# Kernel tuning notes

Hardware: AMD Instinct MI355X
Metric: run time of the kernel (lower is better)

Reference implementation:

```python
import jax, jax.numpy as jnp
import numpy as np

B, S, NQ, H, HD = 2, 4096, 576, 32, 128
HID = H * HD  # 4096


def setup_inputs() -> dict:
    key = jax.random.key(0)
    ks = jax.random.split(key, 7)
    sc = 0.02
    return {
        "hidden_states": jax.random.normal(ks[0], (B, S, HID), jnp.float32),
        "by_pass_hidden_states": jax.random.normal(ks[1], (B, NQ, HID), jnp.float32),
        "attention_mask": jnp.zeros((B, 1, S, NQ), jnp.float32),
        "Wq": jax.random.normal(ks[2], (HID, HID), jnp.float32) * sc,
        "Wk": jax.random.normal(ks[3], (HID, HID), jnp.float32) * sc,
        "Wv": jax.random.normal(ks[4], (HID, HID), jnp.float32) * sc,
        "Wo": jax.random.normal(ks[5], (HID, HID), jnp.float32) * sc,
    }


def reference(hidden_states, by_pass_hidden_states, attention_mask, Wq, Wk, Wv, Wo):
    b, s, _ = hidden_states.shape
    nq = by_pass_hidden_states.shape[1]
    # projections (nn.Linear applies x @ W.T); reshape to (b, heads, len, head_dim)
    q = (hidden_states @ Wq.T).reshape(b, s, H, HD).transpose(0, 2, 1, 3)
    k = (by_pass_hidden_states @ Wk.T).reshape(b, nq, H, HD).transpose(0, 2, 1, 3)
    v = (by_pass_hidden_states @ Wv.T).reshape(b, nq, H, HD).transpose(0, 2, 1, 3)
    # eager QK^T -> mask -> fp32 softmax -> V
    scores = jnp.einsum("bhsd,bhqd->bhsq", q, k) / jnp.sqrt(jnp.float32(HD))
    scores = scores + attention_mask  # (b,1,s,nq) broadcast over heads
    attn = jax.nn.softmax(scores.astype(jnp.float32), axis=-1).astype(q.dtype)
    out = jnp.einsum("bhsq,bhqd->bhsd", attn, v)
    out = out.transpose(0, 2, 1, 3).reshape(b, s, HID)
    return out @ Wo.T
```

## Files before the change

### kernel.cpp

```cpp
#include <hip/hip_runtime.h>
#include <stdint.h>

#define Bn   2
#define Sn   4096
#define NQn  576
#define Hn   32
#define HDn  128
#define HIDn 4096

typedef unsigned short bfu;
typedef short short8 __attribute__((ext_vector_type(8)));
typedef float f32x4 __attribute__((ext_vector_type(4)));

__device__ __forceinline__ bfu f2b(float f) {
  uint32_t x = __builtin_bit_cast(uint32_t, f);
  return (bfu)((x + 0x7fffu + ((x >> 16) & 1u)) >> 16);
}

__device__ __forceinline__ void gload16(const void* g, void* l) {
  __builtin_amdgcn_global_load_lds(
      (const __attribute__((address_space(1))) uint32_t*)g,
      (__attribute__((address_space(3))) uint32_t*)l, 16, 0, 0);
}

__global__ void cast_f32_bf16(const float* __restrict__ in, bfu* __restrict__ out,
                              int n8) {
  int i = blockIdx.x * 256 + threadIdx.x;
  if (i >= n8) return;
  const float4* in4 = (const float4*)in;
  float4 a = in4[2 * i], c = in4[2 * i + 1];
  short8 v;
  v[0] = (short)f2b(a.x); v[1] = (short)f2b(a.y);
  v[2] = (short)f2b(a.z); v[3] = (short)f2b(a.w);
  v[4] = (short)f2b(c.x); v[5] = (short)f2b(c.y);
  v[6] = (short)f2b(c.z); v[7] = (short)f2b(c.w);
  ((short8*)out)[i] = v;
}

template <int WRITE_BF16>
__global__ __launch_bounds__(512, 2)
void gemm_bt256(const bfu* __restrict__ A, const bfu* __restrict__ Bm,
                void* __restrict__ Cout, int M, int N, int K) {
  __shared__ __align__(16) bfu Asm[2][256 * 64];
  __shared__ __align__(16) bfu Bsm[2][256 * 64];
  const int tid = threadIdx.x;
  const int wave = tid >> 6, lane = tid & 63;
  const int lr = lane & 15, kq = lane >> 4;
  const int wm = wave >> 2, wn = wave & 3;
  const long m0 = (long)blockIdx.y * 256, n0 = (long)blockIdx.x * 256;
  const int NT = K >> 6;

  const int c0j = tid >> 3, c0c = tid & 7;
  const int c1j = (512 + tid) >> 3, c1c = tid & 7;
  const bfu* aSrc0 = A + (m0 + c0j) * (long)K + ((c0c ^ (c0j & 7)) * 8);
  const bfu* aSrc1 = A + (m0 + c1j) * (long)K + ((c1c ^ (c1j & 7)) * 8);
  const bfu* bSrc0 = Bm + (n0 + c0j) * (long)K + ((c0c ^ (c0j & 7)) * 8);
  const bfu* bSrc1 = Bm + (n0 + c1j) * (long)K + ((c1c ^ (c1j & 7)) * 8);

  auto stageA = [&](int t, int buf, int half) {
    long koff = (long)t * 64 + (long)half * 128 * K;
    gload16(aSrc0 + koff, &Asm[buf][half * 8192 + (wave * 64) * 8]);
    gload16(aSrc1 + koff, &Asm[buf][half * 8192 + (512 + wave * 64) * 8]);
  };
  auto stageB = [&](int t, int buf, int half) {
    long koff = (long)t * 64 + (long)half * 128 * K;
    gload16(bSrc0 + koff, &Bsm[buf][half * 8192 + (wave * 64) * 8]);
    gload16(bSrc1 + koff, &Bsm[buf][half * 8192 + (512 + wave * 64) * 8]);
  };
  auto ldsA = [&](int buf, int mf, int ks) -> short8 {
    int row = (mf >> 2) * 128 + wm * 64 + (mf & 3) * 16 + lr;
    int off = (row * 128 + ks * 64 + kq * 16) ^ ((row & 7) << 4);
    return *(const short8*)((const char*)Asm[buf] + off);
  };
  auto ldsB = [&](int buf, int nf, int ks) -> short8 {
    int row = (nf >> 1) * 128 + wn * 32 + (nf & 1) * 16 + lr;
    int off = (row * 128 + ks * 64 + kq * 16) ^ ((row & 7) << 4);
    return *(const short8*)((const char*)Bsm[buf] + off);
  };

  f32x4 acc[8][4] = {};

  stageA(0, 0, 0); stageB(0, 0, 0); stageB(0, 0, 1); stageA(0, 0, 1);
  asm volatile("s_waitcnt vmcnt(0)" ::: "memory");
  __builtin_amdgcn_s_barrier();

  for (int t = 0; t < NT; ++t) {
    const int buf = t & 1;
    if (t + 1 < NT) {
      stageA(t + 1, buf ^ 1, 0);
      stageB(t + 1, buf ^ 1, 0);
      stageB(t + 1, buf ^ 1, 1);
      stageA(t + 1, buf ^ 1, 1);
    }
    short8 a0[4][2], a1[4][2], b0[2][2], b1[2][2];
#pragma unroll
    for (int mf = 0; mf < 4; ++mf) {
      a0[mf][0] = ldsA(buf, mf, 0);
      a0[mf][1] = ldsA(buf, mf, 1);
    }
#pragma unroll
    for (int nf = 0; nf < 2; ++nf) {
      b0[nf][0] = ldsB(buf, nf, 0);
      b0[nf][1] = ldsB(buf, nf, 1);
      b1[nf][0] = ldsB(buf, 2 + nf, 0);
      b1[nf][1] = ldsB(buf, 2 + nf, 1);
    }
#pragma unroll
    for (int mf = 0; mf < 4; ++mf)
#pragma unroll
      for (int ks = 0; ks < 2; ++ks)
#pragma unroll
        for (int nf = 0; nf < 2; ++nf)
          acc[mf][nf] = __builtin_amdgcn_mfma_f32_16x16x32_bf16(
              a0[mf][ks], b0[nf][ks], acc[mf][nf], 0, 0, 0);
#pragma unroll
    for (int mf = 0; mf < 4; ++mf) {
      a1[mf][0] = ldsA(buf, 4 + mf, 0);
      a1[mf][1] = ldsA(buf, 4 + mf, 1);
    }
#pragma unroll
    for (int mf = 0; mf < 4; ++mf)
#pragma unroll
      for (int ks = 0; ks < 2; ++ks)
#pragma unroll
        for (int nf = 0; nf < 2; ++nf)
          acc[mf][2 + nf] = __builtin_amdgcn_mfma_f32_16x16x32_bf16(
              a0[mf][ks], b1[nf][ks], acc[mf][2 + nf], 0, 0, 0);
#pragma unroll
    for (int mf = 0; mf < 4; ++mf)
#pragma unroll
      for (int ks = 0; ks < 2; ++ks)
#pragma unroll
        for (int nf = 0; nf < 2; ++nf)
          acc[4 + mf][2 + nf] = __builtin_amdgcn_mfma_f32_16x16x32_bf16(
              a1[mf][ks], b1[nf][ks], acc[4 + mf][2 + nf], 0, 0, 0);
#pragma unroll
    for (int mf = 0; mf < 4; ++mf)
#pragma unroll
      for (int ks = 0; ks < 2; ++ks)
#pragma unroll
        for (int nf = 0; nf < 2; ++nf)
          acc[4 + mf][nf] = __builtin_amdgcn_mfma_f32_16x16x32_bf16(
              a1[mf][ks], b0[nf][ks], acc[4 + mf][nf], 0, 0, 0);
    asm volatile("s_waitcnt vmcnt(0)" ::: "memory");
    __builtin_amdgcn_s_barrier();
  }

#pragma unroll
  for (int mf = 0; mf < 8; ++mf)
#pragma unroll
    for (int nf = 0; nf < 4; ++nf)
#pragma unroll
      for (int r = 0; r < 4; ++r) {
        long row = m0 + (mf >> 2) * 128 + wm * 64 + (mf & 3) * 16 + kq * 4 + r;
        long col = n0 + (nf >> 1) * 128 + wn * 32 + (nf & 1) * 16 + lr;
        float v = acc[mf][nf][r];
        if (WRITE_BF16)
          ((bfu*)Cout)[row * N + col] = f2b(v);
        else
          ((float*)Cout)[row * N + col] = v;
      }
}

template <int WRITE_BF16>
__global__ __launch_bounds__(256, 2)
void gemm_bt(const bfu* __restrict__ A, const bfu* __restrict__ Bm,
             void* __restrict__ Cout, int M, int N, int K) {
  __shared__ __align__(16) bfu As[128 * 32];
  __shared__ __align__(16) bfu Bs[128 * 32];
  const int tid = threadIdx.x;
  const int wave = tid >> 6, lane = tid & 63;
  const int lr = lane & 15, kq = lane >> 4;
  const int wm = wave >> 1, wn = wave & 1;
  const long m0 = (long)blockIdx.y * 128, n0 = (long)blockIdx.x * 128;

  f32x4 acc[4][4] = {};

  for (int kk = 0; kk < K; kk += 32) {
#pragma unroll
    for (int i = 0; i < 2; ++i) {
      int tt = i * 256 + tid;
      long row = tt >> 2;
      int col = (tt & 3) * 8;
      gload16(A + (m0 + row) * K + kk + col, &As[(i * 256 + wave * 64) * 8]);
      gload16(Bm + (n0 + row) * K + kk + col, &Bs[(i * 256 + wave * 64) * 8]);
    }
    __syncthreads();
    short8 a[4], b[4];
#pragma unroll
    for (int mt = 0; mt < 4; ++mt)
      a[mt] = *(const short8*)&As[(wm * 64 + mt * 16 + lr) * 32 + kq * 8];
#pragma unroll
    for (int nt = 0; nt < 4; ++nt)
      b[nt] = *(const short8*)&Bs[(wn * 64 + nt * 16 + lr) * 32 + kq * 8];
#pragma unroll
    for (int mt = 0; mt < 4; ++mt)
#pragma unroll
      for (int nt = 0; nt < 4; ++nt)
        acc[mt][nt] = __builtin_amdgcn_mfma_f32_16x16x32_bf16(
            a[mt], b[nt], acc[mt][nt], 0, 0, 0);
    __syncthreads();
  }
#pragma unroll
  for (int mt = 0; mt < 4; ++mt)
#pragma unroll
    for (int nt = 0; nt < 4; ++nt)
#pragma unroll
      for (int r = 0; r < 4; ++r) {
        long row = m0 + wm * 64 + mt * 16 + kq * 4 + r;
        long col = n0 + wn * 64 + nt * 16 + lr;
        float v = acc[mt][nt][r];
        if (WRITE_BF16)
          ((bfu*)Cout)[row * N + col] = f2b(v);
        else
          ((float*)Cout)[row * N + col] = v;
      }
}

__global__ void transpose_v(const bfu* __restrict__ Vb, bfu* __restrict__ Vt) {
  __shared__ bfu t[32][33];
  const int bh = blockIdx.z;
  const int tq = blockIdx.x;
  const int td = blockIdx.y;
  const int b = bh >> 5, h = bh & 31;
  const int tx = threadIdx.x & 31, ty = threadIdx.x >> 5;
  const bfu* src = Vb + ((long)(b * NQn + tq * 32)) * HIDn + h * HDn + td * 32;
#pragma unroll
  for (int i = 0; i < 32; i += 8) t[ty + i][tx] = src[(long)(ty + i) * HIDn + tx];
  __syncthreads();
  bfu* dst = Vt + ((long)bh * HDn + td * 32) * NQn + tq * 32;
#pragma unroll
  for (int i = 0; i < 32; i += 8) dst[(long)(ty + i) * NQn + tx] = t[tx][ty + i];
}

__global__ __launch_bounds__(256, 3)
void attn_kernel(const bfu* __restrict__ Qb, const bfu* __restrict__ Kb,
                 const bfu* __restrict__ Vt, const float* __restrict__ mask,
                 bfu* __restrict__ AO) {
  __shared__ __align__(16) bfu Ks[2][4096];
  __shared__ __align__(16) bfu Vs[2][4096];
  const int bid = blockIdx.x;
  const int h = bid & (Hn - 1);
  const int b = (bid >> 5) & (Bn - 1);
  const int qt0 = bid >> 6;
  const long q0 = (long)qt0 * 64;
  const int tid = threadIdx.x;
  const int wave = tid >> 6, lane = tid & 63;
  const int lr = lane & 15, kq = lane >> 4;
  const float scale = 0.08838834764831845f;

  const long qrow = (long)b * Sn + q0 + wave * 16 + lr;
  const bfu* Kblk = Kb + (long)b * NQn * HIDn + h * HDn;
  const bfu* Vblk = Vt + ((long)(b * Hn + h)) * HDn * NQn;
  const float* mrow = mask + ((long)b * Sn + q0 + wave * 16 + lr) * NQn;

  auto stageK = [&](int kt, int buf) {
#pragma unroll
    for (int i = 0; i < 2; ++i) {
      int c = i * 256 + tid;
      int j = c >> 4, c16 = c & 15;
      gload16(Kblk + (long)(kt * 32 + j) * HIDn + ((c16 ^ (j & 7)) * 8),
              &Ks[buf][(i * 256 + wave * 64) * 8]);
    }
  };
  auto stageV = [&](int kt, int buf) {
#pragma unroll
    for (int i = 0; i < 2; ++i) {
      int c = i * 256 + tid;
      int j = c >> 2, c4 = c & 3;
      gload16(Vblk + (long)j * NQn + kt * 32 + c4 * 8,
              &Vs[buf][(i * 256 + wave * 64) * 8]);
    }
  };

  stageK(0, 0);
  stageV(0, 0);

  const bfu* Qbase = Qb + qrow * HIDn + h * HDn;
  short8 qf[4];
#pragma unroll
  for (int ks = 0; ks < 4; ++ks)
    qf[ks] = *(const short8*)&Qbase[ks * 32 + kq * 8];

  f32x4 o[8] = {};
  float rsum = 0.f;

  for (int kt = 0; kt < 18; ++kt) {
    __syncthreads();
    const int buf = kt & 1;
    if (kt < 17) {
      stageK(kt + 1, buf ^ 1);
      stageV(kt + 1, buf ^ 1);
    }
    const char* kb = (const char*)Ks[buf];
    f32x4 s0 = {}, s1 = {};
#pragma unroll
    for (int ks = 0; ks < 4; ++ks) {
      short8 kf0 = *(const short8*)(kb + ((lr * 256 + ks * 64 + kq * 16) ^
                                          ((lr & 7) << 4)));
      short8 kf1 = *(const short8*)(kb + (((16 + lr) * 256 + ks * 64 + kq * 16) ^
                                          ((lr & 7) << 4)));
      s0 = __builtin_amdgcn_mfma_f32_16x16x32_bf16(kf0, qf[ks], s0, 0, 0, 0);
      s1 = __builtin_amdgcn_mfma_f32_16x16x32_bf16(kf1, qf[ks], s1, 0, 0, 0);
    }
    float4 m0 = *(const float4*)&mrow[kt * 32 + kq * 4];
    float4 m1 = *(const float4*)&mrow[kt * 32 + 16 + kq * 4];
    float p00 = __expf(s0[0] * scale + m0.x), p01 = __expf(s0[1] * scale + m0.y);
    float p02 = __expf(s0[2] * scale + m0.z), p03 = __expf(s0[3] * scale + m0.w);
    float p10 = __expf(s1[0] * scale + m1.x), p11 = __expf(s1[1] * scale + m1.y);
    float p12 = __expf(s1[2] * scale + m1.z), p13 = __expf(s1[3] * scale + m1.w);
    rsum += ((p00 + p01) + (p02 + p03)) + ((p10 + p11) + (p12 + p13));
    int pk0_0 = (int)((uint32_t)f2b(p00) | ((uint32_t)f2b(p01) << 16));
    int pk0_1 = (int)((uint32_t)f2b(p02) | ((uint32_t)f2b(p03) << 16));
    int pk1_0 = (int)((uint32_t)f2b(p10) | ((uint32_t)f2b(p11) << 16));
    int pk1_1 = (int)((uint32_t)f2b(p12) | ((uint32_t)f2b(p13) << 16));
    const int sLo = lr + (((kq & 1) << 1) << 4);
    const int sHi = sLo + 16;
    int b0, b1, b2, b3;
    {
      int v0 = __shfl(pk0_0, sLo, 64), v1 = __shfl(pk1_0, sLo, 64);
      b0 = (kq < 2) ? v0 : v1;
      v0 = __shfl(pk0_1, sLo, 64); v1 = __shfl(pk1_1, sLo, 64);
      b1 = (kq < 2) ? v0 : v1;
      v0 = __shfl(pk0_0, sHi, 64); v1 = __shfl(pk1_0, sHi, 64);
      b2 = (kq < 2) ? v0 : v1;
      v0 = __shfl(pk0_1, sHi, 64); v1 = __shfl(pk1_1, sHi, 64);
      b3 = (kq < 2) ? v0 : v1;
    }
    int4 pfi = {b0, b1, b2, b3};
    short8 pfrag = __builtin_bit_cast(short8, pfi);
    const char* vb = (const char*)Vs[buf];
#pragma unroll
    for (int dt = 0; dt < 8; ++dt) {
      short8 vf = *(const short8*)(vb + ((dt * 16 + lr) * 64 + kq * 16));
      o[dt] = __builtin_amdgcn_mfma_f32_16x16x32_bf16(vf, pfrag, o[dt], 0, 0, 0);
    }
  }

  rsum += __shfl_xor(rsum, 16, 64);
  rsum += __shfl_xor(rsum, 32, 64);
  const float inv = 1.0f / rsum;

  bfu* Obase = AO + qrow * HIDn + h * HDn;
#pragma unroll
  for (int dt = 0; dt < 8; ++dt) {
    uint64_t pk = (uint64_t)f2b(o[dt][0] * inv) |
                  ((uint64_t)f2b(o[dt][1] * inv) << 16) |
                  ((uint64_t)f2b(o[dt][2] * inv) << 32) |
                  ((uint64_t)f2b(o[dt][3] * inv) << 48);
    *(uint64_t*)&Obase[dt * 16 + kq * 4] = pk;
  }
}

extern "C" void kernel_launch(void* const* d_in, const int* in_sizes, int n_in,
                              void* d_out, int out_size, void* d_ws, size_t ws_size,
                              hipStream_t stream) {
  const float* hs = (const float*)d_in[0];
  const float* bp = (const float*)d_in[1];
  const float* mask = (const float*)d_in[2];
  const float* Wq = (const float*)d_in[3];
  const float* Wk = (const float*)d_in[4];
  const float* Wv = (const float*)d_in[5];
  const float* Wo = (const float*)d_in[6];
  float* out = (float*)d_out;

  const long M1 = (long)Bn * Sn;
  const long M2 = (long)Bn * NQn;
  char* ws = (char*)d_ws;
  bfu* hb = (bfu*)(ws + 0);
  bfu* bb = (bfu*)(ws + 67108864);
  bfu* w1 = (bfu*)(ws + 76546048);
  bfu* wkb = (bfu*)(ws + 110100480);
  bfu* wvb = (bfu*)(ws + 143654912);
  bfu* Qb = (bfu*)(ws + 177209344);
  bfu* Kb = (bfu*)(ws + 244318208);
  bfu* Vb = (bfu*)(ws + 253755392);
  bfu* Vt = (bfu*)(ws + 263192576);

  auto cast = [&](const float* src, bfu* dst, long n) {
    int n8 = (int)(n / 8);
    cast_f32_bf16<<<dim3((n8 + 255) / 256), dim3(256), 0, stream>>>(src, dst, n8);
  };
  cast(hs, hb, M1 * HIDn);
  cast(bp, bb, M2 * HIDn);
  cast(Wq, w1, (long)HIDn * HIDn);
  cast(Wk, wkb, (long)HIDn * HIDn);
  cast(Wv, wvb, (long)HIDn * HIDn);

  gemm_bt256<1><<<dim3(HIDn / 256, M1 / 256), dim3(512), 0, stream>>>(
      hb, w1, Qb, (int)M1, HIDn, HIDn);
  gemm_bt<1><<<dim3(HIDn / 128, M2 / 128), dim3(256), 0, stream>>>(
      bb, wkb, Kb, (int)M2, HIDn, HIDn);
  gemm_bt<1><<<dim3(HIDn / 128, M2 / 128), dim3(256), 0, stream>>>(
      bb, wvb, Vb, (int)M2, HIDn, HIDn);

  cast(Wo, w1, (long)HIDn * HIDn);
  transpose_v<<<dim3(NQn / 32, HDn / 32, Bn * Hn), dim3(256), 0, stream>>>(Vb, Vt);

  attn_kernel<<<dim3((Sn / 64) * Bn * Hn), dim3(256), 0, stream>>>(
      Qb, Kb, Vt, mask, hb );

  gemm_bt256<0><<<dim3(HIDn / 256, M1 / 256), dim3(512), 0, stream>>>(
      hb, w1, out, (int)M1, HIDn, HIDn);
}
```

Measured before the change: 986.3 us.

## Use 32x32x16 MFMA in big GEMM and fuse K/V projections into one GEMM

The 256x256 GEMM now issues 32x32x16 bf16 MFMAs with 16-wide accumulators instead of 16x16x32, which cuts the number of MFMA instructions and changes the LDS fragment layout and epilogue indexing. The K and V projections are merged into a single GEMM against a concatenated [Wk;Wv] weight, producing an interleaved KV buffer with row stride 8192. This saves a launch and improves occupancy for the small-M GEMM. The attention and transpose kernels are updated to read K and V from the fused buffer with the wider stride.

```diff
diff --git a/kernel.cpp b/kernel.cpp
--- a/kernel.cpp
+++ b/kernel.cpp
@@ -11,6 +11,7 @@
 typedef unsigned short bfu;
 typedef short short8 __attribute__((ext_vector_type(8)));
 typedef float f32x4 __attribute__((ext_vector_type(4)));
+typedef float f32x16 __attribute__((ext_vector_type(16)));
 
 __device__ __forceinline__ bfu f2b(float f) {
   uint32_t x = __builtin_bit_cast(uint32_t, f);
@@ -45,7 +46,7 @@
   __shared__ __align__(16) bfu Bsm[2][256 * 64];
   const int tid = threadIdx.x;
   const int wave = tid >> 6, lane = tid & 63;
-  const int lr = lane & 15, kq = lane >> 4;
+  const int l31 = lane & 31, l5 = lane >> 5;
   const int wm = wave >> 2, wn = wave & 3;
   const long m0 = (long)blockIdx.y * 256, n0 = (long)blockIdx.x * 256;
   const int NT = K >> 6;
@@ -68,17 +69,17 @@
     gload16(bSrc1 + koff, &Bsm[buf][half * 8192 + (512 + wave * 64) * 8]);
   };
   auto ldsA = [&](int buf, int mf, int ks) -> short8 {
-    int row = (mf >> 2) * 128 + wm * 64 + (mf & 3) * 16 + lr;
-    int off = (row * 128 + ks * 64 + kq * 16) ^ ((row & 7) << 4);
+    int row = wm * 128 + mf * 32 + l31;
+    int off = (row * 128 + ks * 32 + l5 * 16) ^ ((row & 7) << 4);
     return *(const short8*)((const char*)Asm[buf] + off);
   };
   auto ldsB = [&](int buf, int nf, int ks) -> short8 {
-    int row = (nf >> 1) * 128 + wn * 32 + (nf & 1) * 16 + lr;
-    int off = (row * 128 + ks * 64 + kq * 16) ^ ((row & 7) << 4);
+    int row = nf * 128 + wn * 32 + l31;
+    int off = (row * 128 + ks * 32 + l5 * 16) ^ ((row & 7) << 4);
     return *(const short8*)((const char*)Bsm[buf] + off);
   };
 
-  f32x4 acc[8][4] = {};
+  f32x16 acc[4][2] = {};
 
   stageA(0, 0, 0); stageB(0, 0, 0); stageB(0, 0, 1); stageA(0, 0, 1);
   asm volatile("s_waitcnt vmcnt(0)" ::: "memory");
@@ -92,68 +93,47 @@
       stageB(t + 1, buf ^ 1, 1);
       stageA(t + 1, buf ^ 1, 1);
     }
-    short8 a0[4][2], a1[4][2], b0[2][2], b1[2][2];
-#pragma unroll
-    for (int mf = 0; mf < 4; ++mf) {
-      a0[mf][0] = ldsA(buf, mf, 0);
-      a0[mf][1] = ldsA(buf, mf, 1);
-    }
-#pragma unroll
-    for (int nf = 0; nf < 2; ++nf) {
-      b0[nf][0] = ldsB(buf, nf, 0);
-      b0[nf][1] = ldsB(buf, nf, 1);
-      b1[nf][0] = ldsB(buf, 2 + nf, 0);
-      b1[nf][1] = ldsB(buf, 2 + nf, 1);
-    }
-#pragma unroll
-    for (int mf = 0; mf < 4; ++mf)
-#pragma unroll
-      for (int ks = 0; ks < 2; ++ks)
+    short8 b[2][4], a[2][4];
+#pragma unroll
+    for (int nf = 0; nf < 2; ++nf)
+#pragma unroll
+      for (int ks = 0; ks < 4; ++ks) b[nf][ks] = ldsB(buf, nf, ks);
+#pragma unroll
+    for (int mf = 0; mf < 2; ++mf)
+#pragma unroll
+      for (int ks = 0; ks < 4; ++ks) a[mf][ks] = ldsA(buf, mf, ks);
+#pragma unroll
+    for (int mf = 0; mf < 2; ++mf)
+#pragma unroll
+      for (int ks = 0; ks < 4; ++ks)
 #pragma unroll
         for (int nf = 0; nf < 2; ++nf)
-          acc[mf][nf] = __builtin_amdgcn_mfma_f32_16x16x32_bf16(
-              a0[mf][ks], b0[nf][ks], acc[mf][nf], 0, 0, 0);
-#pragma unroll
-    for (int mf = 0; mf < 4; ++mf) {
-      a1[mf][0] = ldsA(buf, 4 + mf, 0);
-      a1[mf][1] = ldsA(buf, 4 + mf, 1);
-    }
-#pragma unroll
-    for (int mf = 0; mf < 4; ++mf)
-#pragma unroll
-      for (int ks = 0; ks < 2; ++ks)
+          acc[mf][nf] = __builtin_amdgcn_mfma_f32_32x32x16_bf16(
+              a[mf][ks], b[nf][ks], acc[mf][nf], 0, 0, 0);
+#pragma unroll
+    for (int mf = 0; mf < 2; ++mf)
+#pragma unroll
+      for (int ks = 0; ks < 4; ++ks) a[mf][ks] = ldsA(buf, 2 + mf, ks);
+#pragma unroll
+    for (int mf = 0; mf < 2; ++mf)
+#pragma unroll
+      for (int ks = 0; ks < 4; ++ks)
 #pragma unroll
         for (int nf = 0; nf < 2; ++nf)
-          acc[mf][2 + nf] = __builtin_amdgcn_mfma_f32_16x16x32_bf16(
-              a0[mf][ks], b1[nf][ks], acc[mf][2 + nf], 0, 0, 0);
-#pragma unroll
-    for (int mf = 0; mf < 4; ++mf)
-#pragma unroll
-      for (int ks = 0; ks < 2; ++ks)
-#pragma unroll
-        for (int nf = 0; nf < 2; ++nf)
-          acc[4 + mf][2 + nf] = __builtin_amdgcn_mfma_f32_16x16x32_bf16(
-              a1[mf][ks], b1[nf][ks], acc[4 + mf][2 + nf], 0, 0, 0);
-#pragma unroll
-    for (int mf = 0; mf < 4; ++mf)
-#pragma unroll
-      for (int ks = 0; ks < 2; ++ks)
-#pragma unroll
-        for (int nf = 0; nf < 2; ++nf)
-          acc[4 + mf][nf] = __builtin_amdgcn_mfma_f32_16x16x32_bf16(
-              a1[mf][ks], b0[nf][ks], acc[4 + mf][nf], 0, 0, 0);
+          acc[2 + mf][nf] = __builtin_amdgcn_mfma_f32_32x32x16_bf16(
+              a[mf][ks], b[nf][ks], acc[2 + mf][nf], 0, 0, 0);
     asm volatile("s_waitcnt vmcnt(0)" ::: "memory");
     __builtin_amdgcn_s_barrier();
   }
 
 #pragma unroll
-  for (int mf = 0; mf < 8; ++mf)
-#pragma unroll
-    for (int nf = 0; nf < 4; ++nf)
-#pragma unroll
-      for (int r = 0; r < 4; ++r) {
-        long row = m0 + (mf >> 2) * 128 + wm * 64 + (mf & 3) * 16 + kq * 4 + r;
-        long col = n0 + (nf >> 1) * 128 + wn * 32 + (nf & 1) * 16 + lr;
+  for (int mf = 0; mf < 4; ++mf)
+#pragma unroll
+    for (int nf = 0; nf < 2; ++nf)
+#pragma unroll
+      for (int r = 0; r < 16; ++r) {
+        long row = m0 + wm * 128 + mf * 32 + (r & 3) + 8 * (r >> 2) + 4 * l5;
+        long col = n0 + nf * 128 + wn * 32 + l31;
         float v = acc[mf][nf][r];
         if (WRITE_BF16)
           ((bfu*)Cout)[row * N + col] = f2b(v);
@@ -217,16 +197,17 @@
       }
 }
 
-__global__ void transpose_v(const bfu* __restrict__ Vb, bfu* __restrict__ Vt) {
+__global__ void transpose_v(const bfu* __restrict__ KVb, bfu* __restrict__ Vt) {
   __shared__ bfu t[32][33];
   const int bh = blockIdx.z;
   const int tq = blockIdx.x;
   const int td = blockIdx.y;
   const int b = bh >> 5, h = bh & 31;
   const int tx = threadIdx.x & 31, ty = threadIdx.x >> 5;
-  const bfu* src = Vb + ((long)(b * NQn + tq * 32)) * HIDn + h * HDn + td * 32;
-#pragma unroll
-  for (int i = 0; i < 32; i += 8) t[ty + i][tx] = src[(long)(ty + i) * HIDn + tx];
+  const bfu* src =
+      KVb + ((long)(b * NQn + tq * 32)) * 8192 + 4096 + h * HDn + td * 32;
+#pragma unroll
+  for (int i = 0; i < 32; i += 8) t[ty + i][tx] = src[(long)(ty + i) * 8192 + tx];
   __syncthreads();
   bfu* dst = Vt + ((long)bh * HDn + td * 32) * NQn + tq * 32;
 #pragma unroll
@@ -234,7 +215,7 @@
 }
 
 __global__ __launch_bounds__(256, 3)
-void attn_kernel(const bfu* __restrict__ Qb, const bfu* __restrict__ Kb,
+void attn_kernel(const bfu* __restrict__ Qb, const bfu* __restrict__ KVb,
                  const bfu* __restrict__ Vt, const float* __restrict__ mask,
                  bfu* __restrict__ AO) {
   __shared__ __align__(16) bfu Ks[2][4096];
@@ -250,7 +231,7 @@
   const float scale = 0.08838834764831845f;
 
   const long qrow = (long)b * Sn + q0 + wave * 16 + lr;
-  const bfu* Kblk = Kb + (long)b * NQn * HIDn + h * HDn;
+  const bfu* Kblk = KVb + (long)b * NQn * 8192 + h * HDn;
   const bfu* Vblk = Vt + ((long)(b * Hn + h)) * HDn * NQn;
   const float* mrow = mask + ((long)b * Sn + q0 + wave * 16 + lr) * NQn;
 
@@ -259,7 +240,7 @@
     for (int i = 0; i < 2; ++i) {
       int c = i * 256 + tid;
       int j = c >> 4, c16 = c & 15;
-      gload16(Kblk + (long)(kt * 32 + j) * HIDn + ((c16 ^ (j & 7)) * 8),
+      gload16(Kblk + (long)(kt * 32 + j) * 8192 + ((c16 ^ (j & 7)) * 8),
               &Ks[buf][(i * 256 + wave * 64) * 8]);
     }
   };
@@ -370,11 +351,9 @@
   bfu* hb = (bfu*)(ws + 0);
   bfu* bb = (bfu*)(ws + 67108864);
   bfu* w1 = (bfu*)(ws + 76546048);
-  bfu* wkb = (bfu*)(ws + 110100480);
-  bfu* wvb = (bfu*)(ws + 143654912);
+  bfu* wkv = (bfu*)(ws + 110100480);
   bfu* Qb = (bfu*)(ws + 177209344);
-  bfu* Kb = (bfu*)(ws + 244318208);
-  bfu* Vb = (bfu*)(ws + 253755392);
+  bfu* KVb = (bfu*)(ws + 244318208);
   bfu* Vt = (bfu*)(ws + 263192576);
 
   auto cast = [&](const float* src, bfu* dst, long n) {
@@ -384,21 +363,20 @@
   cast(hs, hb, M1 * HIDn);
   cast(bp, bb, M2 * HIDn);
   cast(Wq, w1, (long)HIDn * HIDn);
-  cast(Wk, wkb, (long)HIDn * HIDn);
-  cast(Wv, wvb, (long)HIDn * HIDn);
+  cast(Wk, wkv, (long)HIDn * HIDn);
+  cast(Wv, wkv + (long)HIDn * HIDn, (long)HIDn * HIDn);
 
   gemm_bt256<1><<<dim3(HIDn / 256, M1 / 256), dim3(512), 0, stream>>>(
       hb, w1, Qb, (int)M1, HIDn, HIDn);
-  gemm_bt<1><<<dim3(HIDn / 128, M2 / 128), dim3(256), 0, stream>>>(
-      bb, wkb, Kb, (int)M2, HIDn, HIDn);
-  gemm_bt<1><<<dim3(HIDn / 128, M2 / 128), dim3(256), 0, stream>>>(
-      bb, wvb, Vb, (int)M2, HIDn, HIDn);
+  gemm_bt<1><<<dim3(8192 / 128, M2 / 128), dim3(256), 0, stream>>>(
+      bb, wkv, KVb, (int)M2, 8192, HIDn);
 
   cast(Wo, w1, (long)HIDn * HIDn);
-  transpose_v<<<dim3(NQn / 32, HDn / 32, Bn * Hn), dim3(256), 0, stream>>>(Vb, Vt);
+  transpose_v<<<dim3(NQn / 32, HDn / 32, Bn * Hn), dim3(256), 0, stream>>>(
+      KVb, Vt);
 
   attn_kernel<<<dim3((Sn / 64) * Bn * Hn), dim3(256), 0, stream>>>(
-      Qb, Kb, Vt, mask, hb );
+      Qb, KVb, Vt, mask, hb );
 
   gemm_bt256<0><<<dim3(HIDn / 256, M1 / 256), dim3(512), 0, stream>>>(
       hb, w1, out, (int)M1, HIDn, HIDn);
```

After: 951.2 us. 3.6% less time.
